# Performance work log

Measured on AMD Instinct MI355X. Metric: run time of the kernel, lower is better.

## Reference

```python
import jax, jax.numpy as jnp
import numpy as np

B, S, L, D = 64, 512, 6, 512  # batch, seq_len, densely_layer_num, feature dim


def setup_inputs() -> dict:
    key = jax.random.key(0)
    ks = jax.random.split(key, L + 1)
    inp = {f"x{j}": jax.random.normal(ks[j], (B, S, D), dtype=jnp.float32) for j in range(L)}
    # keras initializers.get('normal') -> RandomNormal(stddev=0.05)
    inp["Ws"] = jax.random.normal(ks[L], (S, L, L), dtype=jnp.float32) * 0.05
    return inp


def reference(x0, x1, x2, x3, x4, x5, Ws):
    # Stack densely-connected layer outputs: [B, S, L, D]
    X = jnp.stack([x0, x1, x2, x3, x4, x5], axis=2)
    # Per-position summary over feature dim: [B, S, L]
    s = jnp.sum(X, axis=-1)
    # Per-position (L x L) projection, softmax over layer axis
    logits = jnp.einsum('bsl,slm->bsm', s, Ws)  # [B, S, L]
    a = jax.nn.softmax(logits, axis=-1)
    # Attention-weighted sum over layers: [B, S, D]
    return jnp.einsum('bsl,bsld->bsd', a, X)
```

## Files before the change

### kernel.cpp

```cpp
#include <hip/hip_runtime.h>

constexpr int Bc = 64, Sc = 512, Lc = 6, Dc = 512;

__global__ __launch_bounds__(256) void densely_att_kernel(
    const float* __restrict__ x0, const float* __restrict__ x1,
    const float* __restrict__ x2, const float* __restrict__ x3,
    const float* __restrict__ x4, const float* __restrict__ x5,
    const float* __restrict__ Ws, float* __restrict__ out)
{
    const int wave = threadIdx.x >> 6;
    const int lane = threadIdx.x & 63;
    const long pos = (long)blockIdx.x * 4 + wave;

    const int s_idx = __builtin_amdgcn_readfirstlane((int)(pos % Sc));

    const float* xs[Lc] = {x0, x1, x2, x3, x4, x5};

    const size_t base0 = (size_t)pos * Dc + (size_t)lane * 4;
    const size_t base1 = base0 + 256;

    float4 v[Lc][2];
    float ssum[Lc];
    #pragma unroll
    for (int j = 0; j < Lc; ++j) {
        v[j][0] = *(const float4*)(xs[j] + base0);
        v[j][1] = *(const float4*)(xs[j] + base1);
        ssum[j] = (v[j][0].x + v[j][0].y) + (v[j][0].z + v[j][0].w)
                + (v[j][1].x + v[j][1].y) + (v[j][1].z + v[j][1].w);
    }

    #pragma unroll
    for (int off = 32; off >= 1; off >>= 1) {
        #pragma unroll
        for (int j = 0; j < Lc; ++j)
            ssum[j] += __shfl_xor(ssum[j], off, 64);
    }

    const float* __restrict__ w = Ws + (size_t)s_idx * (Lc * Lc);
    float logits[Lc];
    #pragma unroll
    for (int m = 0; m < Lc; ++m) {
        float acc = 0.f;
        #pragma unroll
        for (int l = 0; l < Lc; ++l)
            acc = fmaf(ssum[l], w[l * Lc + m], acc);
        logits[m] = acc;
    }

    float mx = logits[0];
    #pragma unroll
    for (int m = 1; m < Lc; ++m) mx = fmaxf(mx, logits[m]);
    float a[Lc];
    float denom = 0.f;
    #pragma unroll
    for (int m = 0; m < Lc; ++m) {
        a[m] = __expf(logits[m] - mx);
        denom += a[m];
    }
    const float inv = 1.f / denom;
    #pragma unroll
    for (int m = 0; m < Lc; ++m) a[m] *= inv;

    float4 o0 = make_float4(0.f, 0.f, 0.f, 0.f);
    float4 o1 = make_float4(0.f, 0.f, 0.f, 0.f);
    #pragma unroll
    for (int j = 0; j < Lc; ++j) {
        o0.x = fmaf(a[j], v[j][0].x, o0.x);
        o0.y = fmaf(a[j], v[j][0].y, o0.y);
        o0.z = fmaf(a[j], v[j][0].z, o0.z);
        o0.w = fmaf(a[j], v[j][0].w, o0.w);
        o1.x = fmaf(a[j], v[j][1].x, o1.x);
        o1.y = fmaf(a[j], v[j][1].y, o1.y);
        o1.z = fmaf(a[j], v[j][1].z, o1.z);
        o1.w = fmaf(a[j], v[j][1].w, o1.w);
    }
    *(float4*)(out + base0) = o0;
    *(float4*)(out + base1) = o1;
}

extern "C" void kernel_launch(void* const* d_in, const int* in_sizes, int n_in,
                              void* d_out, int out_size, void* d_ws, size_t ws_size,
                              hipStream_t stream) {
    const float* x0 = (const float*)d_in[0];
    const float* x1 = (const float*)d_in[1];
    const float* x2 = (const float*)d_in[2];
    const float* x3 = (const float*)d_in[3];
    const float* x4 = (const float*)d_in[4];
    const float* x5 = (const float*)d_in[5];
    const float* Ws = (const float*)d_in[6];
    float* out = (float*)d_out;

    const int positions = Bc * Sc;
    const int blocks = positions / 4;
    densely_att_kernel<<<blocks, 256, 0, stream>>>(x0, x1, x2, x3, x4, x5, Ws, out);
}
```

Baseline: 356.0 us.

## Split each position across two waves with LDS sum combine

```diff
diff --git a/kernel.cpp b/kernel.cpp
--- a/kernel.cpp
+++ b/kernel.cpp
@@ -1,6 +1,8 @@
 #include <hip/hip_runtime.h>
 
 constexpr int Bc = 64, Sc = 512, Lc = 6, Dc = 512;
+
+#define KEEP4(v) asm volatile("" : "+v"((v).x), "+v"((v).y), "+v"((v).z), "+v"((v).w))
 
 __global__ __launch_bounds__(256) void densely_att_kernel(
     const float* __restrict__ x0, const float* __restrict__ x1,
@@ -10,23 +12,23 @@
 {
     const int wave = threadIdx.x >> 6;
     const int lane = threadIdx.x & 63;
-    const long pos = (long)blockIdx.x * 4 + wave;
+    const int pair = wave >> 1;
+    const int half = wave & 1;
 
+    const long pos = (long)blockIdx.x * 2 + pair;
     const int s_idx = __builtin_amdgcn_readfirstlane((int)(pos % Sc));
 
     const float* xs[Lc] = {x0, x1, x2, x3, x4, x5};
 
-    const size_t base0 = (size_t)pos * Dc + (size_t)lane * 4;
-    const size_t base1 = base0 + 256;
+    const size_t base = (size_t)pos * Dc + (size_t)half * 256 + (size_t)lane * 4;
 
-    float4 v[Lc][2];
+    float4 v[Lc];
     float ssum[Lc];
     #pragma unroll
     for (int j = 0; j < Lc; ++j) {
-        v[j][0] = *(const float4*)(xs[j] + base0);
-        v[j][1] = *(const float4*)(xs[j] + base1);
-        ssum[j] = (v[j][0].x + v[j][0].y) + (v[j][0].z + v[j][0].w)
-                + (v[j][1].x + v[j][1].y) + (v[j][1].z + v[j][1].w);
+        v[j] = *(const float4*)(xs[j] + base);
+        KEEP4(v[j]);
+        ssum[j] = (v[j].x + v[j].y) + (v[j].z + v[j].w);
     }
 
     #pragma unroll
@@ -35,6 +37,16 @@
         for (int j = 0; j < Lc; ++j)
             ssum[j] += __shfl_xor(ssum[j], off, 64);
     }
+
+    __shared__ float sums[2][2][Lc];
+    if (lane == 0) {
+        #pragma unroll
+        for (int j = 0; j < Lc; ++j) sums[pair][half][j] = ssum[j];
+    }
+    __syncthreads();
+    #pragma unroll
+    for (int j = 0; j < Lc; ++j)
+        ssum[j] = sums[pair][0][j] + sums[pair][1][j];
 
     const float* __restrict__ w = Ws + (size_t)s_idx * (Lc * Lc);
     float logits[Lc];
@@ -61,21 +73,15 @@
     #pragma unroll
     for (int m = 0; m < Lc; ++m) a[m] *= inv;
 
-    float4 o0 = make_float4(0.f, 0.f, 0.f, 0.f);
-    float4 o1 = make_float4(0.f, 0.f, 0.f, 0.f);
+    float4 o = make_float4(0.f, 0.f, 0.f, 0.f);
     #pragma unroll
     for (int j = 0; j < Lc; ++j) {
-        o0.x = fmaf(a[j], v[j][0].x, o0.x);
-        o0.y = fmaf(a[j], v[j][0].y, o0.y);
-        o0.z = fmaf(a[j], v[j][0].z, o0.z);
-        o0.w = fmaf(a[j], v[j][0].w, o0.w);
-        o1.x = fmaf(a[j], v[j][1].x, o1.x);
-        o1.y = fmaf(a[j], v[j][1].y, o1.y);
-        o1.z = fmaf(a[j], v[j][1].z, o1.z);
-        o1.w = fmaf(a[j], v[j][1].w, o1.w);
+        o.x = fmaf(a[j], v[j].x, o.x);
+        o.y = fmaf(a[j], v[j].y, o.y);
+        o.z = fmaf(a[j], v[j].z, o.z);
+        o.w = fmaf(a[j], v[j].w, o.w);
     }
-    *(float4*)(out + base0) = o0;
-    *(float4*)(out + base1) = o1;
+    *(float4*)(out + base) = o;
 }
 
 extern "C" void kernel_launch(void* const* d_in, const int* in_sizes, int n_in,
@@ -91,6 +97,6 @@
     float* out = (float*)d_out;
 
     const int positions = Bc * Sc;
-    const int blocks = positions / 4;
+    const int blocks = positions / 2;
     densely_att_kernel<<<blocks, 256, 0, stream>>>(x0, x1, x2, x3, x4, x5, Ws, out);
 }
```

Measured after the change: 351.1 us. No clear change (-1.4%).
